# Performance work log

Measured on AMD Instinct MI355X. Metric: run time of the kernel, lower is better.

The kernel has to match this reference:

```python
import jax, jax.numpy as jnp
import numpy as np

EPS = 1e-8  # torch nn.CosineSimilarity default eps


def setup_inputs() -> dict:
    key = jax.random.key(0)
    k1, k2, k3 = jax.random.split(key, 3)
    N, K, Q, CH, H, W, D = 32, 5, 15, 3, 84, 84, 1600
    supp_x = jax.random.normal(k1, (N, K, CH, H, W), dtype=jnp.float32)
    query_x = jax.random.normal(k2, (N, Q, CH, H, W), dtype=jnp.float32)
    W_enc = jax.random.normal(k3, (CH * H * W, D), dtype=jnp.float32) * 0.02
    return {"supp_x": supp_x, "query_x": query_x, "W_enc": W_enc}


def reference(supp_x, query_x, W_enc):
    N, K = supp_x.shape[0], supp_x.shape[1]
    Q = query_x.shape[1]
    # encoder: flatten image -> linear projection (stands in for backbone)
    s_feat = supp_x.reshape(N * K, -1) @ W_enc          # (N*K, D)
    x_proto = s_feat.reshape(N, K, -1).mean(axis=1)     # (N, D) class prototypes
    x_q = query_x.reshape(N * Q, -1) @ W_enc            # (N*Q, D)
    # cosine similarity: L2-normalize with eps clamp, then single matmul
    qn = x_q / jnp.maximum(jnp.linalg.norm(x_q, axis=1, keepdims=True), EPS)
    pn = x_proto / jnp.maximum(jnp.linalg.norm(x_proto, axis=1, keepdims=True), EPS)
    sim = qn @ pn.T                                     # (N*Q, N)
    return jax.nn.log_softmax(sim, axis=1)
```

## Files before the change

kernel.cpp:

```cpp
#include <hip/hip_runtime.h>
#include <cstdint>
#include <cstddef>

namespace {

constexpr int NCLS   = 32;
constexpr int KSHOT  = 5;
constexpr int FDIM   = 21168;
constexpr int KPAD   = 21248;
constexpr int DDIM   = 1600;
constexpr int NROW   = 512;
constexpr int NQROW  = 480;
constexpr int NKT    = 332;
constexpr int SPLITK = 16;
constexpr int CHUNK  = 21;

using short8 = __attribute__((ext_vector_type(8))) short;
using f32x4  = __attribute__((ext_vector_type(4))) float;

__device__ __forceinline__ unsigned short f2bf(float x) {
    union { float f; unsigned u; } v; v.f = x;
    unsigned r = v.u + 0x7fffu + ((v.u >> 16) & 1u);
    return (unsigned short)(r >> 16);
}

__global__ void prep_A(const float* __restrict__ supp,
                       const float* __restrict__ query,
                       unsigned short* __restrict__ A) {
    const int units = NROW * (KPAD / 4);
    for (int u = blockIdx.x * blockDim.x + threadIdx.x; u < units;
         u += gridDim.x * blockDim.x) {
        const int r = u / (KPAD / 4);
        const int c = (u % (KPAD / 4)) * 4;
        float4 v = make_float4(0.f, 0.f, 0.f, 0.f);
        if (c < FDIM) {
            if (r < NCLS) {
                const float* s = supp + (size_t)r * KSHOT * FDIM + c;
                float4 a0 = *(const float4*)(s);
                float4 a1 = *(const float4*)(s + FDIM);
                float4 a2 = *(const float4*)(s + 2 * FDIM);
                float4 a3 = *(const float4*)(s + 3 * FDIM);
                float4 a4 = *(const float4*)(s + 4 * FDIM);
                v.x = (a0.x + a1.x + a2.x + a3.x + a4.x) * 0.2f;
                v.y = (a0.y + a1.y + a2.y + a3.y + a4.y) * 0.2f;
                v.z = (a0.z + a1.z + a2.z + a3.z + a4.z) * 0.2f;
                v.w = (a0.w + a1.w + a2.w + a3.w + a4.w) * 0.2f;
            } else {
                v = *(const float4*)(query + (size_t)(r - NCLS) * FDIM + c);
            }
        }
        ushort4 o;
        o.x = f2bf(v.x); o.y = f2bf(v.y); o.z = f2bf(v.z); o.w = f2bf(v.w);
        *(ushort4*)(A + (size_t)r * KPAD + c) = o;
    }
}

__global__ __launch_bounds__(512, 4) void gemm_kernel(
        const unsigned short* __restrict__ A,
        const float* __restrict__ W,
        float* __restrict__ Cpart) {
    __shared__ unsigned short Al[256 * 64];
    __shared__ unsigned short Bl[128 * 72];

    const int b   = blockIdx.x;
    const int s   = b / 26;
    const int rem = b % 26;
    const int mt  = rem / 13;
    const int nt  = rem % 13;
    const int m0  = mt * 256;
    const int n0  = nt * 128;
    const int t0  = s * CHUNK;
    const int t1  = min(NKT, t0 + CHUNK);

    const int tid  = threadIdx.x;
    const int lane = tid & 63;
    const int wid  = tid >> 6;
    const int wr   = wid >> 1;
    const int wc   = wid & 1;

    const int bn = tid & 127;
    const int bw = tid >> 7;
    const int ncol = n0 + bn;
    const bool nok = ncol < DDIM;

    const int arow_in_chunk = lane >> 3;
    const int ablk = lane & 7;

    f32x4 acc[4][4];
    #pragma unroll
    for (int i = 0; i < 4; ++i)
        #pragma unroll
        for (int j = 0; j < 4; ++j)
            acc[i][j] = (f32x4){0.f, 0.f, 0.f, 0.f};

    for (int t = t0; t < t1; ++t) {
        const int k0 = t * 64;
        #pragma unroll
        for (int i = 0; i < 4; ++i) {
            const int rowbase = (wid * 4 + i) * 8;
            const int row = rowbase + arow_in_chunk;
            const int d = ablk ^ (row & 7);
            const unsigned short* src =
                A + (size_t)(m0 + row) * KPAD + k0 + d * 8;
            unsigned short* dst = &Al[rowbase * 64];
            __builtin_amdgcn_global_load_lds(
                (const __attribute__((address_space(1))) void*)src,
                (__attribute__((address_space(3))) void*)dst, 16, 0, 0);
        }
        #pragma unroll
        for (int half = 0; half < 2; ++half) {
            const int kb = k0 + bw * 16 + half * 8;
            unsigned short h[8];
            #pragma unroll
            for (int i = 0; i < 8; ++i) {
                const int kg = kb + i;
                float v = (nok && kg < FDIM) ? W[(size_t)kg * DDIM + ncol] : 0.f;
                h[i] = f2bf(v);
            }
            uint4 pk;
            pk.x = (unsigned)h[0] | ((unsigned)h[1] << 16);
            pk.y = (unsigned)h[2] | ((unsigned)h[3] << 16);
            pk.z = (unsigned)h[4] | ((unsigned)h[5] << 16);
            pk.w = (unsigned)h[6] | ((unsigned)h[7] << 16);
            *(uint4*)(&Bl[bn * 72 + bw * 16 + half * 8]) = pk;
        }
        __syncthreads();
        #pragma unroll
        for (int kk = 0; kk < 2; ++kk) {
            short8 af[4], bfr[4];
            #pragma unroll
            for (int ms = 0; ms < 4; ++ms) {
                const int R = wr * 64 + ms * 16 + (lane & 15);
                const int dd = kk * 4 + (lane >> 4);
                const int pos = dd ^ (R & 7);
                af[ms] = *(const short8*)(&Al[R * 64 + pos * 8]);
            }
            #pragma unroll
            for (int ns = 0; ns < 4; ++ns) {
                const int Rn = wc * 64 + ns * 16 + (lane & 15);
                bfr[ns] = *(const short8*)(&Bl[Rn * 72 + kk * 32 + (lane >> 4) * 8]);
            }
            #pragma unroll
            for (int ms = 0; ms < 4; ++ms)
                #pragma unroll
                for (int ns = 0; ns < 4; ++ns)
                    acc[ms][ns] = __builtin_amdgcn_mfma_f32_16x16x32_bf16(
                        af[ms], bfr[ns], acc[ms][ns], 0, 0, 0);
        }
        __syncthreads();
    }

    float* Cp = Cpart + (size_t)s * NROW * DDIM;
    #pragma unroll
    for (int ms = 0; ms < 4; ++ms) {
        const int row = m0 + wr * 64 + ms * 16 + ((lane >> 4) * 4);
        #pragma unroll
        for (int ns = 0; ns < 4; ++ns) {
            const int col = n0 + wc * 64 + ns * 16 + (lane & 15);
            if (col < DDIM) {
                #pragma unroll
                for (int r = 0; r < 4; ++r)
                    Cp[(size_t)(row + r) * DDIM + col] = acc[ms][ns][r];
            }
        }
    }
}

__global__ void reduce_norm(const float* __restrict__ Cpart,
                            float* __restrict__ C,
                            float* __restrict__ inv_norm) {
    const int row = blockIdx.x;
    const int tid = threadIdx.x;
    float acc = 0.f;
    for (int c = tid; c < DDIM; c += 256) {
        float v = 0.f;
        #pragma unroll
        for (int s2 = 0; s2 < SPLITK; ++s2)
            v += Cpart[(size_t)s2 * NROW * DDIM + (size_t)row * DDIM + c];
        C[(size_t)row * DDIM + c] = v;
        acc += v * v;
    }
    __shared__ float red[4];
    #pragma unroll
    for (int off = 32; off > 0; off >>= 1) acc += __shfl_xor(acc, off);
    if ((tid & 63) == 0) red[tid >> 6] = acc;
    __syncthreads();
    if (tid == 0) {
        float a = red[0] + red[1] + red[2] + red[3];
        inv_norm[row] = 1.f / fmaxf(sqrtf(a), 1e-8f);
    }
}

__global__ void simlog(const float* __restrict__ C,
                       const float* __restrict__ inv_norm,
                       float* __restrict__ out) {
    __shared__ float qs[DDIM];
    __shared__ float sims[NCLS];
    const int r = blockIdx.x;
    const int tid = threadIdx.x;
    const float* qrow = C + (size_t)(NCLS + r) * DDIM;
    for (int c = tid; c < DDIM; c += 256) qs[c] = qrow[c];
    __syncthreads();
    const float invq = inv_norm[NCLS + r];
    const int lane = tid & 63, w = tid >> 6;
    #pragma unroll
    for (int j = 0; j < 8; ++j) {
        const int p = w * 8 + j;
        const float* prow = C + (size_t)p * DDIM;
        float d = 0.f;
        for (int c = lane; c < DDIM; c += 64) d += qs[c] * prow[c];
        #pragma unroll
        for (int off = 32; off > 0; off >>= 1) d += __shfl_xor(d, off);
        if (lane == 0) sims[p] = d * invq * inv_norm[p];
    }
    __syncthreads();
    if (w == 0) {
        float v = (lane < NCLS) ? sims[lane] : -1e30f;
        float m = v;
        #pragma unroll
        for (int off = 32; off > 0; off >>= 1) m = fmaxf(m, __shfl_xor(m, off));
        float e = (lane < NCLS) ? expf(v - m) : 0.f;
        float ss = e;
        #pragma unroll
        for (int off = 32; off > 0; off >>= 1) ss += __shfl_xor(ss, off);
        if (lane < NCLS) out[(size_t)r * NCLS + lane] = v - m - logf(ss);
    }
}

}


extern "C" void kernel_launch(void* const* d_in, const int* in_sizes, int n_in,
                              void* d_out, int out_size, void* d_ws, size_t ws_size,
                              hipStream_t stream) {
    const float* supp  = (const float*)d_in[0];
    const float* query = (const float*)d_in[1];
    const float* Wenc  = (const float*)d_in[2];
    float* out = (float*)d_out;

    char* ws = (char*)d_ws;
    unsigned short* A = (unsigned short*)ws;
    float* Cpart     = (float*)(ws + 21757952);
    float* C         = (float*)(ws + 21757952 + 52428800);
    float* inv_norm  = (float*)(ws + 21757952 + 52428800 + 3276800);

    hipLaunchKernelGGL(prep_A, dim3(2048), dim3(256), 0, stream, supp, query, A);
    hipLaunchKernelGGL(gemm_kernel, dim3(SPLITK * 26), dim3(512), 0, stream,
                       A, Wenc, Cpart);
    hipLaunchKernelGGL(reduce_norm, dim3(NROW), dim3(256), 0, stream,
                       Cpart, C, inv_norm);
    hipLaunchKernelGGL(simlog, dim3(NQROW), dim3(256), 0, stream,
                       C, inv_norm, out);
}
```

Before: 161.2 us.

## Restructure GEMM to full-M tiles with register A loads and double-buffered B

```diff
diff --git a/kernel.cpp b/kernel.cpp
--- a/kernel.cpp
+++ b/kernel.cpp
@@ -12,16 +12,24 @@
 constexpr int NROW   = 512;
 constexpr int NQROW  = 480;
 constexpr int NKT    = 332;
-constexpr int SPLITK = 16;
-constexpr int CHUNK  = 21;
+constexpr int MAXS   = 19;
 
 using short8 = __attribute__((ext_vector_type(8))) short;
 using f32x4  = __attribute__((ext_vector_type(4))) float;
 
-__device__ __forceinline__ unsigned short f2bf(float x) {
+__device__ __forceinline__ unsigned f2bf(float x) {
     union { float f; unsigned u; } v; v.f = x;
     unsigned r = v.u + 0x7fffu + ((v.u >> 16) & 1u);
-    return (unsigned short)(r >> 16);
+    return r >> 16;
+}
+
+__device__ __forceinline__ uint4 pack8(const float* v) {
+    uint4 p;
+    p.x = f2bf(v[0]) | (f2bf(v[1]) << 16);
+    p.y = f2bf(v[2]) | (f2bf(v[3]) << 16);
+    p.z = f2bf(v[4]) | (f2bf(v[5]) << 16);
+    p.w = f2bf(v[6]) | (f2bf(v[7]) << 16);
+    return p;
 }
 
 __global__ void prep_A(const float* __restrict__ supp,
@@ -50,113 +58,117 @@
             }
         }
         ushort4 o;
-        o.x = f2bf(v.x); o.y = f2bf(v.y); o.z = f2bf(v.z); o.w = f2bf(v.w);
+        o.x = (unsigned short)f2bf(v.x); o.y = (unsigned short)f2bf(v.y);
+        o.z = (unsigned short)f2bf(v.z); o.w = (unsigned short)f2bf(v.w);
         *(ushort4*)(A + (size_t)r * KPAD + c) = o;
     }
 }
 
-__global__ __launch_bounds__(512, 4) void gemm_kernel(
+__global__ __launch_bounds__(512, 2) void gemm2(
         const unsigned short* __restrict__ A,
         const float* __restrict__ W,
-        float* __restrict__ Cpart) {
-    __shared__ unsigned short Al[256 * 64];
-    __shared__ unsigned short Bl[128 * 72];
-
-    const int b   = blockIdx.x;
-    const int s   = b / 26;
-    const int rem = b % 26;
-    const int mt  = rem / 13;
-    const int nt  = rem % 13;
-    const int m0  = mt * 256;
-    const int n0  = nt * 128;
-    const int t0  = s * CHUNK;
-    const int t1  = min(NKT, t0 + CHUNK);
+        float* __restrict__ Cpart, int S) {
+    __shared__ unsigned short Bl[2][128 * 64];
+
+    const int b  = blockIdx.x;
+    const int nt = b % 13;
+    const int s  = b / 13;
+    const int n0 = nt * 128;
+    const int t0 = (NKT * s) / S;
+    const int t1 = (NKT * (s + 1)) / S;
 
     const int tid  = threadIdx.x;
     const int lane = tid & 63;
     const int wid  = tid >> 6;
-    const int wr   = wid >> 1;
-    const int wc   = wid & 1;
+    const int g    = lane >> 4;
+    const int r15  = lane & 15;
 
     const int bn = tid & 127;
     const int bw = tid >> 7;
     const int ncol = n0 + bn;
     const bool nok = ncol < DDIM;
-
-    const int arow_in_chunk = lane >> 3;
-    const int ablk = lane & 7;
-
-    f32x4 acc[4][4];
+    const float* Wp = W + ncol;
+    const int woff0 = bn * 64 + (((bw * 2 + 0) ^ (bn & 7)) * 8);
+    const int woff1 = bn * 64 + (((bw * 2 + 1) ^ (bn & 7)) * 8);
+
+    const unsigned short* Arow[4];
+    #pragma unroll
+    for (int ms = 0; ms < 4; ++ms)
+        Arow[ms] = A + (size_t)(wid * 64 + ms * 16 + r15) * KPAD + g * 8;
+
+    f32x4 acc[4][8];
     #pragma unroll
     for (int i = 0; i < 4; ++i)
         #pragma unroll
-        for (int j = 0; j < 4; ++j)
+        for (int j = 0; j < 8; ++j)
             acc[i][j] = (f32x4){0.f, 0.f, 0.f, 0.f};
 
+    {
+        const int k0 = t0 * 64;
+        float wv[16];
+        #pragma unroll
+        for (int i = 0; i < 16; ++i) {
+            const int kg = k0 + bw * 16 + i;
+            wv[i] = (nok && kg < FDIM) ? Wp[(size_t)kg * DDIM] : 0.f;
+        }
+        *(uint4*)(&Bl[0][woff0]) = pack8(wv);
+        *(uint4*)(&Bl[0][woff1]) = pack8(wv + 8);
+    }
+    __syncthreads();
+
+    int cur = 0;
     for (int t = t0; t < t1; ++t) {
         const int k0 = t * 64;
-        #pragma unroll
-        for (int i = 0; i < 4; ++i) {
-            const int rowbase = (wid * 4 + i) * 8;
-            const int row = rowbase + arow_in_chunk;
-            const int d = ablk ^ (row & 7);
-            const unsigned short* src =
-                A + (size_t)(m0 + row) * KPAD + k0 + d * 8;
-            unsigned short* dst = &Al[rowbase * 64];
-            __builtin_amdgcn_global_load_lds(
-                (const __attribute__((address_space(1))) void*)src,
-                (__attribute__((address_space(3))) void*)dst, 16, 0, 0);
-        }
-        #pragma unroll
-        for (int half = 0; half < 2; ++half) {
-            const int kb = k0 + bw * 16 + half * 8;
-            unsigned short h[8];
-            #pragma unroll
-            for (int i = 0; i < 8; ++i) {
-                const int kg = kb + i;
-                float v = (nok && kg < FDIM) ? W[(size_t)kg * DDIM + ncol] : 0.f;
-                h[i] = f2bf(v);
-            }
-            uint4 pk;
-            pk.x = (unsigned)h[0] | ((unsigned)h[1] << 16);
-            pk.y = (unsigned)h[2] | ((unsigned)h[3] << 16);
-            pk.z = (unsigned)h[4] | ((unsigned)h[5] << 16);
-            pk.w = (unsigned)h[6] | ((unsigned)h[7] << 16);
-            *(uint4*)(&Bl[bn * 72 + bw * 16 + half * 8]) = pk;
-        }
-        __syncthreads();
+        short8 af[2][4];
+        #pragma unroll
+        for (int kk = 0; kk < 2; ++kk)
+            #pragma unroll
+            for (int ms = 0; ms < 4; ++ms)
+                af[kk][ms] = *(const short8*)(Arow[ms] + k0 + kk * 32);
+
+        const bool more = (t + 1 < t1);
+        float wv[16];
+        if (more) {
+            const int kn = k0 + 64;
+            #pragma unroll
+            for (int i = 0; i < 16; ++i) {
+                const int kg = kn + bw * 16 + i;
+                wv[i] = (nok && kg < FDIM) ? Wp[(size_t)kg * DDIM] : 0.f;
+            }
+        }
+
         #pragma unroll
         for (int kk = 0; kk < 2; ++kk) {
-            short8 af[4], bfr[4];
-            #pragma unroll
-            for (int ms = 0; ms < 4; ++ms) {
-                const int R = wr * 64 + ms * 16 + (lane & 15);
-                const int dd = kk * 4 + (lane >> 4);
-                const int pos = dd ^ (R & 7);
-                af[ms] = *(const short8*)(&Al[R * 64 + pos * 8]);
-            }
-            #pragma unroll
-            for (int ns = 0; ns < 4; ++ns) {
-                const int Rn = wc * 64 + ns * 16 + (lane & 15);
-                bfr[ns] = *(const short8*)(&Bl[Rn * 72 + kk * 32 + (lane >> 4) * 8]);
+            short8 bfr[8];
+            #pragma unroll
+            for (int ns = 0; ns < 8; ++ns) {
+                const int Rn  = ns * 16 + r15;
+                const int pos = (kk * 4 + g) ^ (Rn & 7);
+                bfr[ns] = *(const short8*)(&Bl[cur][Rn * 64 + pos * 8]);
             }
             #pragma unroll
             for (int ms = 0; ms < 4; ++ms)
                 #pragma unroll
-                for (int ns = 0; ns < 4; ++ns)
+                for (int ns = 0; ns < 8; ++ns)
                     acc[ms][ns] = __builtin_amdgcn_mfma_f32_16x16x32_bf16(
-                        af[ms], bfr[ns], acc[ms][ns], 0, 0, 0);
+                        af[kk][ms], bfr[ns], acc[ms][ns], 0, 0, 0);
+        }
+
+        if (more) {
+            *(uint4*)(&Bl[cur ^ 1][woff0]) = pack8(wv);
+            *(uint4*)(&Bl[cur ^ 1][woff1]) = pack8(wv + 8);
         }
         __syncthreads();
+        cur ^= 1;
     }
 
     float* Cp = Cpart + (size_t)s * NROW * DDIM;
     #pragma unroll
     for (int ms = 0; ms < 4; ++ms) {
-        const int row = m0 + wr * 64 + ms * 16 + ((lane >> 4) * 4);
-        #pragma unroll
-        for (int ns = 0; ns < 4; ++ns) {
-            const int col = n0 + wc * 64 + ns * 16 + (lane & 15);
+        const int row = wid * 64 + ms * 16 + g * 4;
+        #pragma unroll
+        for (int ns = 0; ns < 8; ++ns) {
+            const int col = n0 + ns * 16 + r15;
             if (col < DDIM) {
                 #pragma unroll
                 for (int r = 0; r < 4; ++r)
@@ -168,15 +180,14 @@
 
 __global__ void reduce_norm(const float* __restrict__ Cpart,
                             float* __restrict__ C,
-                            float* __restrict__ inv_norm) {
+                            float* __restrict__ inv_norm, int S) {
     const int row = blockIdx.x;
     const int tid = threadIdx.x;
     float acc = 0.f;
     for (int c = tid; c < DDIM; c += 256) {
         float v = 0.f;
-        #pragma unroll
-        for (int s2 = 0; s2 < SPLITK; ++s2)
-            v += Cpart[(size_t)s2 * NROW * DDIM + (size_t)row * DDIM + c];
+        for (int s2 = 0; s2 < S; ++s2)
+            v += Cpart[((size_t)s2 * NROW + row) * DDIM + c];
         C[(size_t)row * DDIM + c] = v;
         acc += v * v;
     }
@@ -238,17 +249,24 @@
     const float* Wenc  = (const float*)d_in[2];
     float* out = (float*)d_out;
 
+    const size_t slot   = (size_t)NROW * DDIM * 4;
+    const size_t fixedA = (size_t)NROW * KPAD * 2;
+    int S = MAXS;
+    if (ws_size) {
+        while (S > 1 && fixedA + (size_t)S * slot + slot + 4096 > ws_size) --S;
+    }
+
     char* ws = (char*)d_ws;
     unsigned short* A = (unsigned short*)ws;
-    float* Cpart     = (float*)(ws + 21757952);
-    float* C         = (float*)(ws + 21757952 + 52428800);
-    float* inv_norm  = (float*)(ws + 21757952 + 52428800 + 3276800);
+    float* Cpart    = (float*)(ws + fixedA);
+    float* C        = (float*)(ws + fixedA + (size_t)S * slot);
+    float* inv_norm = (float*)(ws + fixedA + (size_t)(S + 1) * slot);
 
     hipLaunchKernelGGL(prep_A, dim3(2048), dim3(256), 0, stream, supp, query, A);
-    hipLaunchKernelGGL(gemm_kernel, dim3(SPLITK * 26), dim3(512), 0, stream,
-                       A, Wenc, Cpart);
+    hipLaunchKernelGGL(gemm2, dim3(13 * S), dim3(512), 0, stream,
+                       A, Wenc, Cpart, S);
     hipLaunchKernelGGL(reduce_norm, dim3(NROW), dim3(256), 0, stream,
-                       Cpart, C, inv_norm);
+                       Cpart, C, inv_norm, S);
     hipLaunchKernelGGL(simlog, dim3(NQROW), dim3(256), 0, stream,
                        C, inv_norm, out);
 }
```

New measurement: 190.9 us. +18.4%, slower.

## Pre-transpose weights to bf16 and load both GEMM operands via direct-to-LDS

Applied to the files above, without the earlier changes.

```diff
diff --git a/kernel.cpp b/kernel.cpp
--- a/kernel.cpp
+++ b/kernel.cpp
@@ -12,8 +12,7 @@
 constexpr int NROW   = 512;
 constexpr int NQROW  = 480;
 constexpr int NKT    = 332;
-constexpr int SPLITK = 16;
-constexpr int CHUNK  = 21;
+constexpr int MAXS   = 14;
 
 using short8 = __attribute__((ext_vector_type(8))) short;
 using f32x4  = __attribute__((ext_vector_type(4))) float;
@@ -27,64 +26,105 @@
 __global__ void prep_A(const float* __restrict__ supp,
                        const float* __restrict__ query,
                        unsigned short* __restrict__ A) {
-    const int units = NROW * (KPAD / 4);
-    for (int u = blockIdx.x * blockDim.x + threadIdx.x; u < units;
-         u += gridDim.x * blockDim.x) {
-        const int r = u / (KPAD / 4);
-        const int c = (u % (KPAD / 4)) * 4;
-        float4 v = make_float4(0.f, 0.f, 0.f, 0.f);
-        if (c < FDIM) {
-            if (r < NCLS) {
-                const float* s = supp + (size_t)r * KSHOT * FDIM + c;
-                float4 a0 = *(const float4*)(s);
-                float4 a1 = *(const float4*)(s + FDIM);
-                float4 a2 = *(const float4*)(s + 2 * FDIM);
-                float4 a3 = *(const float4*)(s + 3 * FDIM);
-                float4 a4 = *(const float4*)(s + 4 * FDIM);
-                v.x = (a0.x + a1.x + a2.x + a3.x + a4.x) * 0.2f;
-                v.y = (a0.y + a1.y + a2.y + a3.y + a4.y) * 0.2f;
-                v.z = (a0.z + a1.z + a2.z + a3.z + a4.z) * 0.2f;
-                v.w = (a0.w + a1.w + a2.w + a3.w + a4.w) * 0.2f;
-            } else {
-                v = *(const float4*)(query + (size_t)(r - NCLS) * FDIM + c);
-            }
-        }
-        ushort4 o;
-        o.x = f2bf(v.x); o.y = f2bf(v.y); o.z = f2bf(v.z); o.w = f2bf(v.w);
-        *(ushort4*)(A + (size_t)r * KPAD + c) = o;
-    }
-}
-
-__global__ __launch_bounds__(512, 4) void gemm_kernel(
+    const int r = blockIdx.y;
+    const int u = blockIdx.x * blockDim.x + threadIdx.x;
+    if (u >= KPAD / 4) return;
+    const int c = u * 4;
+    float4 v = make_float4(0.f, 0.f, 0.f, 0.f);
+    if (c < FDIM) {
+        if (r < NCLS) {
+            const float* s = supp + (size_t)r * KSHOT * FDIM + c;
+            float4 a0 = *(const float4*)(s);
+            float4 a1 = *(const float4*)(s + FDIM);
+            float4 a2 = *(const float4*)(s + 2 * FDIM);
+            float4 a3 = *(const float4*)(s + 3 * FDIM);
+            float4 a4 = *(const float4*)(s + 4 * FDIM);
+            v.x = (a0.x + a1.x + a2.x + a3.x + a4.x) * 0.2f;
+            v.y = (a0.y + a1.y + a2.y + a3.y + a4.y) * 0.2f;
+            v.z = (a0.z + a1.z + a2.z + a3.z + a4.z) * 0.2f;
+            v.w = (a0.w + a1.w + a2.w + a3.w + a4.w) * 0.2f;
+        } else {
+            v = *(const float4*)(query + (size_t)(r - NCLS) * FDIM + c);
+        }
+    }
+    ushort4 o;
+    o.x = f2bf(v.x); o.y = f2bf(v.y); o.z = f2bf(v.z); o.w = f2bf(v.w);
+    *(ushort4*)(A + (size_t)r * KPAD + c) = o;
+}
+
+__global__ void prep_Wt(const float* __restrict__ W,
+                        unsigned short* __restrict__ Wt) {
+    __shared__ unsigned short T[64][68];
+    const int k0 = blockIdx.x * 64;
+    const int n0 = blockIdx.y * 64;
+    const int t  = threadIdx.x;
+    const int cr = t >> 4;
+    const int cc = (t & 15) * 4;
+    #pragma unroll
+    for (int p = 0; p < 4; ++p) {
+        const int kr = p * 16 + cr;
+        const int kg = k0 + kr;
+        float4 v = (kg < FDIM)
+                 ? *(const float4*)&W[(size_t)kg * DDIM + n0 + cc]
+                 : make_float4(0.f, 0.f, 0.f, 0.f);
+        T[cc + 0][kr] = f2bf(v.x);
+        T[cc + 1][kr] = f2bf(v.y);
+        T[cc + 2][kr] = f2bf(v.z);
+        T[cc + 3][kr] = f2bf(v.w);
+    }
+    __syncthreads();
+    #pragma unroll
+    for (int p = 0; p < 2; ++p) {
+        const int nr = p * 32 + (t >> 3);
+        const int ks = (t & 7) * 8;
+        uint2 lo = *(const uint2*)&T[nr][ks];
+        uint2 hi = *(const uint2*)&T[nr][ks + 4];
+        *(uint4*)&Wt[(size_t)(n0 + nr) * KPAD + k0 + ks] =
+            make_uint4(lo.x, lo.y, hi.x, hi.y);
+    }
+}
+
+__global__ __launch_bounds__(256, 3) void gemm4(
         const unsigned short* __restrict__ A,
-        const float* __restrict__ W,
-        float* __restrict__ Cpart) {
-    __shared__ unsigned short Al[256 * 64];
-    __shared__ unsigned short Bl[128 * 72];
-
-    const int b   = blockIdx.x;
-    const int s   = b / 26;
-    const int rem = b % 26;
+        const unsigned short* __restrict__ Wt,
+        float* __restrict__ Cpart, int S) {
+    __shared__ unsigned short Al[128 * 64];
+    __shared__ unsigned short Bl[128 * 64];
+
+    const int bid = blockIdx.x;
+    const int s   = bid / 52;
+    const int rem = bid % 52;
     const int mt  = rem / 13;
     const int nt  = rem % 13;
-    const int m0  = mt * 256;
+    const int m0  = mt * 128;
     const int n0  = nt * 128;
-    const int t0  = s * CHUNK;
-    const int t1  = min(NKT, t0 + CHUNK);
+    const int t0  = (NKT * s) / S;
+    const int t1  = (NKT * (s + 1)) / S;
 
     const int tid  = threadIdx.x;
     const int lane = tid & 63;
-    const int wid  = tid >> 6;
-    const int wr   = wid >> 1;
-    const int wc   = wid & 1;
-
-    const int bn = tid & 127;
-    const int bw = tid >> 7;
-    const int ncol = n0 + bn;
-    const bool nok = ncol < DDIM;
-
-    const int arow_in_chunk = lane >> 3;
-    const int ablk = lane & 7;
+    const int w    = tid >> 6;
+    const int wr   = w & 1;
+    const int wc   = w >> 1;
+    const int r15  = lane & 15;
+    const int g    = lane >> 4;
+    const int srow = lane >> 3;
+    const int sblk = lane & 7;
+
+    const unsigned short* Asrc[4];
+    const unsigned short* Bsrc[4];
+    unsigned short* Adst[4];
+    unsigned short* Bdst[4];
+    #pragma unroll
+    for (int i = 0; i < 4; ++i) {
+        const int r = w * 32 + i * 8 + srow;
+        const int d = (sblk ^ (r & 7)) * 8;
+        Asrc[i] = A + (size_t)(m0 + r) * KPAD + d;
+        const int bn = min(n0 + r, DDIM - 1);
+        Bsrc[i] = Wt + (size_t)bn * KPAD + d;
+        Adst[i] = &Al[(w * 32 + i * 8) * 64];
+        Bdst[i] = &Bl[(w * 32 + i * 8) * 64];
+    }
 
     f32x4 acc[4][4];
     #pragma unroll
@@ -97,55 +137,33 @@
         const int k0 = t * 64;
         #pragma unroll
         for (int i = 0; i < 4; ++i) {
-            const int rowbase = (wid * 4 + i) * 8;
-            const int row = rowbase + arow_in_chunk;
-            const int d = ablk ^ (row & 7);
-            const unsigned short* src =
-                A + (size_t)(m0 + row) * KPAD + k0 + d * 8;
-            unsigned short* dst = &Al[rowbase * 64];
             __builtin_amdgcn_global_load_lds(
-                (const __attribute__((address_space(1))) void*)src,
-                (__attribute__((address_space(3))) void*)dst, 16, 0, 0);
-        }
-        #pragma unroll
-        for (int half = 0; half < 2; ++half) {
-            const int kb = k0 + bw * 16 + half * 8;
-            unsigned short h[8];
-            #pragma unroll
-            for (int i = 0; i < 8; ++i) {
-                const int kg = kb + i;
-                float v = (nok && kg < FDIM) ? W[(size_t)kg * DDIM + ncol] : 0.f;
-                h[i] = f2bf(v);
-            }
-            uint4 pk;
-            pk.x = (unsigned)h[0] | ((unsigned)h[1] << 16);
-            pk.y = (unsigned)h[2] | ((unsigned)h[3] << 16);
-            pk.z = (unsigned)h[4] | ((unsigned)h[5] << 16);
-            pk.w = (unsigned)h[6] | ((unsigned)h[7] << 16);
-            *(uint4*)(&Bl[bn * 72 + bw * 16 + half * 8]) = pk;
+                (const __attribute__((address_space(1))) void*)(Asrc[i] + k0),
+                (__attribute__((address_space(3))) void*)Adst[i], 16, 0, 0);
+            __builtin_amdgcn_global_load_lds(
+                (const __attribute__((address_space(1))) void*)(Bsrc[i] + k0),
+                (__attribute__((address_space(3))) void*)Bdst[i], 16, 0, 0);
         }
         __syncthreads();
         #pragma unroll
         for (int kk = 0; kk < 2; ++kk) {
-            short8 af[4], bfr[4];
+            short8 af[4], bf[4];
             #pragma unroll
             for (int ms = 0; ms < 4; ++ms) {
-                const int R = wr * 64 + ms * 16 + (lane & 15);
-                const int dd = kk * 4 + (lane >> 4);
-                const int pos = dd ^ (R & 7);
-                af[ms] = *(const short8*)(&Al[R * 64 + pos * 8]);
+                const int R = wr * 64 + ms * 16 + r15;
+                af[ms] = *(const short8*)&Al[R * 64 + (((kk * 4 + g) ^ (R & 7)) * 8)];
             }
             #pragma unroll
             for (int ns = 0; ns < 4; ++ns) {
-                const int Rn = wc * 64 + ns * 16 + (lane & 15);
-                bfr[ns] = *(const short8*)(&Bl[Rn * 72 + kk * 32 + (lane >> 4) * 8]);
+                const int Rn = wc * 64 + ns * 16 + r15;
+                bf[ns] = *(const short8*)&Bl[Rn * 64 + (((kk * 4 + g) ^ (Rn & 7)) * 8)];
             }
             #pragma unroll
             for (int ms = 0; ms < 4; ++ms)
                 #pragma unroll
                 for (int ns = 0; ns < 4; ++ns)
                     acc[ms][ns] = __builtin_amdgcn_mfma_f32_16x16x32_bf16(
-                        af[ms], bfr[ns], acc[ms][ns], 0, 0, 0);
+                        af[ms], bf[ns], acc[ms][ns], 0, 0, 0);
         }
         __syncthreads();
     }
@@ -153,10 +171,10 @@
     float* Cp = Cpart + (size_t)s * NROW * DDIM;
     #pragma unroll
     for (int ms = 0; ms < 4; ++ms) {
-        const int row = m0 + wr * 64 + ms * 16 + ((lane >> 4) * 4);
+        const int row = m0 + wr * 64 + ms * 16 + g * 4;
         #pragma unroll
         for (int ns = 0; ns < 4; ++ns) {
-            const int col = n0 + wc * 64 + ns * 16 + (lane & 15);
+            const int col = n0 + wc * 64 + ns * 16 + r15;
             if (col < DDIM) {
                 #pragma unroll
                 for (int r = 0; r < 4; ++r)
@@ -168,15 +186,14 @@
 
 __global__ void reduce_norm(const float* __restrict__ Cpart,
                             float* __restrict__ C,
-                            float* __restrict__ inv_norm) {
+                            float* __restrict__ inv_norm, int S) {
     const int row = blockIdx.x;
     const int tid = threadIdx.x;
     float acc = 0.f;
     for (int c = tid; c < DDIM; c += 256) {
         float v = 0.f;
-        #pragma unroll
-        for (int s2 = 0; s2 < SPLITK; ++s2)
-            v += Cpart[(size_t)s2 * NROW * DDIM + (size_t)row * DDIM + c];
+        for (int s2 = 0; s2 < S; ++s2)
+            v += Cpart[((size_t)s2 * NROW + row) * DDIM + c];
         C[(size_t)row * DDIM + c] = v;
         acc += v * v;
     }
@@ -238,17 +255,32 @@
     const float* Wenc  = (const float*)d_in[2];
     float* out = (float*)d_out;
 
+    const size_t offWt = 21757952;
+    const size_t offCp = offWt + 67993600;
+    const size_t slot  = (size_t)NROW * DDIM * 4;
+
+    int S = MAXS;
+    if (ws_size > offCp) {
+        size_t avail = (ws_size - offCp) / slot;
+        if ((size_t)S > avail) S = (int)avail;
+    }
+    if (S < 1) S = 1;
+
     char* ws = (char*)d_ws;
-    unsigned short* A = (unsigned short*)ws;
-    float* Cpart     = (float*)(ws + 21757952);
-    float* C         = (float*)(ws + 21757952 + 52428800);
-    float* inv_norm  = (float*)(ws + 21757952 + 52428800 + 3276800);
-
-    hipLaunchKernelGGL(prep_A, dim3(2048), dim3(256), 0, stream, supp, query, A);
-    hipLaunchKernelGGL(gemm_kernel, dim3(SPLITK * 26), dim3(512), 0, stream,
-                       A, Wenc, Cpart);
+    unsigned short* A  = (unsigned short*)ws;
+    unsigned short* Wt = (unsigned short*)(ws + offWt);
+    float* Cpart    = (float*)(ws + offCp);
+    float* C        = (float*)(ws + offWt);
+    float* inv_norm = (float*)(ws + offWt + slot);
+
+    hipLaunchKernelGGL(prep_A, dim3((KPAD / 4 + 255) / 256, NROW), dim3(256),
+                       0, stream, supp, query, A);
+    hipLaunchKernelGGL(prep_Wt, dim3(KPAD / 64, DDIM / 64), dim3(256),
+                       0, stream, Wenc, Wt);
+    hipLaunchKernelGGL(gemm4, dim3(52 * S), dim3(256), 0, stream,
+                       A, Wt, Cpart, S);
     hipLaunchKernelGGL(reduce_norm, dim3(NROW), dim3(256), 0, stream,
-                       Cpart, C, inv_norm);
+                       Cpart, C, inv_norm, S);
     hipLaunchKernelGGL(simlog, dim3(NQROW), dim3(256), 0, stream,
                        C, inv_norm, out);
 }
```

Result: slower. 221.3 us (+37.3%).
